# Kernel tuning notes

Measured on AMD Instinct MI355X. Metric: run time of the kernel, lower is better.

## Reference

```python
import jax, jax.numpy as jnp
import numpy as np

EPS = 1e-5
NUM_HEADS = 12

def _ln(x, g, b):
    m = jnp.mean(x, -1, keepdims=True)
    v = jnp.var(x, -1, keepdims=True)
    return (x - m) * jax.lax.rsqrt(v + EPS) * g + b

def setup_inputs():
    key = jax.random.key(0)
    ks = jax.random.split(key, 8)
    D, Dh = 768, 3072
    B, T, H, Wd = 8, 8, 14, 14
    def w(k, shape, scale=0.02):
        return jax.random.normal(k, shape, jnp.float32) * scale
    return dict(
        x=jax.random.normal(ks[0], (B, T * H * Wd + 1, D), jnp.float32),
        W_mq=w(ks[1], (D, D)), b_mq=jnp.zeros((D,), jnp.float32),
        W_mk=w(ks[2], (D, D)), b_mk=jnp.zeros((D,), jnp.float32),
        g1=jnp.ones((D,), jnp.float32), be1=jnp.zeros((D,), jnp.float32),
        W_qkv=w(ks[3], (3 * D, D)),
        W_proj=w(ks[4], (D, D)), b_proj=jnp.zeros((D,), jnp.float32),
        g2=jnp.ones((D,), jnp.float32), be2=jnp.zeros((D,), jnp.float32),
        W_fc1=w(ks[5], (Dh, D)), b_fc1=jnp.zeros((Dh,), jnp.float32),
        W_fc2=w(ks[6], (D, Dh)), b_fc2=jnp.zeros((D,), jnp.float32),
        B=B, T=T, H=H, Wd=Wd,
    )

def reference(x, W_mq, b_mq, W_mk, b_mk, g1, be1, W_qkv, W_proj, b_proj,
              g2, be2, W_fc1, b_fc1, W_fc2, b_fc2, B, T, H, Wd):
    D = x.shape[-1]
    nh = NUM_HEADS
    hd = D // nh
    res = x
    # cls token: (B,1,D) -> repeated per frame -> (B*T,1,D)
    cls = jnp.repeat(x[:, :1, :], T, axis=1).reshape(B * T, 1, D)
    # spatial tokens: 'b (h w t) m -> (b t) (h w) m'  (t is fastest-varying)
    xs = x[:, 1:, :].reshape(B, H * Wd, T, D).transpose(0, 2, 1, 3).reshape(B * T, H * Wd, D)
    xt = jnp.concatenate([cls, xs], axis=1)  # (BT, N=197, D)
    # learned QK-gated mask
    qm = xt @ W_mq.T + b_mq
    km = xt @ W_mk.T + b_mk
    lm = jnp.einsum('bnd,bmd->bnm', qm, km)
    lm = lm.at[:, 0, 0].set(100.0)  # force cls->cls gate open
    lm = jax.nn.sigmoid(lm)
    # attention (drop rates are 0; drop_path is identity at inference)
    xn = _ln(xt, g1, be1)
    BT, N = xt.shape[0], xt.shape[1]
    qkv = (xn @ W_qkv.T).reshape(BT, N, 3, nh, hd).transpose(2, 0, 3, 1, 4)
    q, k, v = qkv[0], qkv[1], qkv[2]  # (BT, nh, N, hd)
    attn = jax.nn.softmax(jnp.einsum('bhnd,bhmd->bhnm', q, k) * (hd ** -0.5), axis=-1)
    attn = attn * lm[:, None, :, :]  # gate attention probs with learned mask
    o = jnp.einsum('bhnm,bhmd->bhnd', attn, v).transpose(0, 2, 1, 3).reshape(BT, N, D)
    o = o @ W_proj.T + b_proj
    # gather cls back (mean over frames) and scatter tokens back
    cls_o = jnp.mean(o[:, 0, :].reshape(B, T, D), axis=1, keepdims=True)  # (B,1,D)
    xs_o = o[:, 1:, :].reshape(B, T, H * Wd, D).transpose(0, 2, 1, 3).reshape(B, H * Wd * T, D)
    y = res + jnp.concatenate([cls_o, xs_o], axis=1)
    # MLP
    h = _ln(y, g2, be2)
    h = jax.nn.gelu(h @ W_fc1.T + b_fc1, approximate=False)
    y = y + (h @ W_fc2.T + b_fc2)
    return (y, lm)
```

## Files before the change

### kernel.cpp

```cpp
#include <hip/hip_runtime.h>
#include <cstdint>

typedef _Float16 f16;
typedef f16 f16x2 __attribute__((ext_vector_type(2)));
typedef f16 f16x4 __attribute__((ext_vector_type(4)));
typedef f16 f16x8 __attribute__((ext_vector_type(8)));
typedef float f32x4 __attribute__((ext_vector_type(4)));

constexpr int D = 768;
constexpr int NTOK = 197;
constexpr int BT = 64;
constexpr int ROWS_A = BT * NTOK;
constexpr int SEQ = 1569;
constexpr int ROWS_Y = 8 * SEQ;
constexpr int DH = 3072;
constexpr int CW = 2304;
constexpr long Y_ELEMS = (long)ROWS_Y * D;
constexpr long LM_ELEMS = (long)BT * NTOK * NTOK;

__device__ __forceinline__ void gload_lds16(const f16* g, f16* l) {
  __builtin_amdgcn_global_load_lds(
      (const __attribute__((address_space(1))) void*)g,
      (__attribute__((address_space(3))) void*)l, 16, 0, 0);
}

__global__ __launch_bounds__(256) void cvt_f16(const float* __restrict__ in,
                                               f16* __restrict__ out, int n4) {
  int i = blockIdx.x * 256 + threadIdx.x;
  if (i >= n4) return;
  const float4 v = *(const float4*)(in + (size_t)i * 4);
  f16x4 o = {(f16)v.x, (f16)v.y, (f16)v.z, (f16)v.w};
  *(f16x4*)(out + (size_t)i * 4) = o;
}

__global__ __launch_bounds__(192) void build_xt_xn(
    const float* __restrict__ x, const float* __restrict__ g1,
    const float* __restrict__ be1, f16* __restrict__ xt, f16* __restrict__ xn) {
  const int rid = blockIdx.x;
  const int bt = rid / NTOK, n = rid % NTOK;
  const int b = bt >> 3, t = bt & 7;
  const int src = (n == 0) ? b * SEQ : b * SEQ + 1 + (n - 1) * 8 + t;
  const int tid = threadIdx.x, d0 = tid * 4;
  const float4 v = *(const float4*)(x + (size_t)src * D + d0);
  float s = v.x + v.y + v.z + v.w;
  float q = v.x * v.x + v.y * v.y + v.z * v.z + v.w * v.w;
  const int lane = tid & 63, wv = tid >> 6;
  for (int off = 32; off; off >>= 1) {
    s += __shfl_xor(s, off);
    q += __shfl_xor(q, off);
  }
  __shared__ float red[2][3];
  if (lane == 0) { red[0][wv] = s; red[1][wv] = q; }
  __syncthreads();
  s = red[0][0] + red[0][1] + red[0][2];
  q = red[1][0] + red[1][1] + red[1][2];
  const float mean = s * (1.f / 768.f);
  const float var = q * (1.f / 768.f) - mean * mean;
  const float rs = rsqrtf(var + 1e-5f);
  const size_t ob = (size_t)rid * D + d0;
  f16x4 xo = {(f16)v.x, (f16)v.y, (f16)v.z, (f16)v.w};
  *(f16x4*)(xt + ob) = xo;
  const float4 gv = *(const float4*)(g1 + d0);
  const float4 bv = *(const float4*)(be1 + d0);
  f16x4 no = {(f16)((v.x - mean) * rs * gv.x + bv.x),
              (f16)((v.y - mean) * rs * gv.y + bv.y),
              (f16)((v.z - mean) * rs * gv.z + bv.z),
              (f16)((v.w - mean) * rs * gv.w + bv.w)};
  *(f16x4*)(xn + ob) = no;
}

constexpr int EPI_F16 = 0;
constexpr int EPI_F16_BIAS = 1;
constexpr int EPI_SIG = 2;
constexpr int EPI_F16_BIAS_GELU = 3;
constexpr int EPI_F32_BIAS_RES = 4;

template <int EPI>
__global__ __launch_bounds__(256, 3) void gemm_f16(
    const f16* __restrict__ A, const f16* __restrict__ B,
    const float* __restrict__ bias, float* __restrict__ Cf,
    f16* __restrict__ Ch, const float* __restrict__ Res, int M, int N, int K,
    int ldc, long sA, long sB, long sC) {
  constexpr int BM = 128, BN = 128, BK = 32;
  __shared__ f16 As[BM][BK];
  __shared__ f16 Bs[BN][BK];
  const int tid = threadIdx.x;
  const int bm = blockIdx.y * BM, bn = blockIdx.x * BN;
  const int z = blockIdx.z;
  A += (size_t)z * sA;
  B += (size_t)z * sB;
  const int lane = tid & 63, wave = tid >> 6;
  const int wm = (wave >> 1) * 64, wn = (wave & 1) * 64;
  const int l15 = lane & 15, quad = lane >> 4;

  const int gr = lane >> 2;
  const int gc = (lane & 3) * 8;
  int a_row0 = bm + wave * 16 + gr;       if (a_row0 >= M) a_row0 = M - 1;
  int a_row1 = bm + (wave + 4) * 16 + gr; if (a_row1 >= M) a_row1 = M - 1;
  int b_row0 = bn + wave * 16 + gr;       if (b_row0 >= N) b_row0 = N - 1;
  int b_row1 = bn + (wave + 4) * 16 + gr; if (b_row1 >= N) b_row1 = N - 1;
  const f16* ap0 = A + (size_t)a_row0 * K + gc;
  const f16* ap1 = A + (size_t)a_row1 * K + gc;
  const f16* bp0 = B + (size_t)b_row0 * K + gc;
  const f16* bp1 = B + (size_t)b_row1 * K + gc;
  f16* as0 = &As[wave * 16][0];
  f16* as1 = &As[(wave + 4) * 16][0];
  f16* bs0 = &Bs[wave * 16][0];
  f16* bs1 = &Bs[(wave + 4) * 16][0];

  f32x4 acc[4][4] = {};

  for (int kt = 0; kt < K; kt += BK) {
    gload_lds16(ap0 + kt, as0);
    gload_lds16(ap1 + kt, as1);
    gload_lds16(bp0 + kt, bs0);
    gload_lds16(bp1 + kt, bs1);
    __syncthreads();
    f16x8 af[4], bf[4];
#pragma unroll
    for (int i = 0; i < 4; i++) {
      af[i] = *(const f16x8*)&As[wm + i * 16 + l15][quad * 8];
      bf[i] = *(const f16x8*)&Bs[wn + i * 16 + l15][quad * 8];
    }
#pragma unroll
    for (int i = 0; i < 4; i++)
#pragma unroll
      for (int j = 0; j < 4; j++)
        acc[i][j] =
            __builtin_amdgcn_mfma_f32_16x16x32_f16(af[i], bf[j], acc[i][j], 0, 0, 0);
    __syncthreads();
  }

#pragma unroll
  for (int i = 0; i < 4; i++) {
#pragma unroll
    for (int j = 0; j < 4; j++) {
      const int col = bn + wn + j * 16 + l15;
      if (col >= N) continue;
#pragma unroll
      for (int r = 0; r < 4; r++) {
        const int row = bm + wm + i * 16 + quad * 4 + r;
        if (row >= M) continue;
        float v = acc[i][j][r];
        const size_t ci = (size_t)z * sC + (size_t)row * ldc + col;
        if constexpr (EPI == EPI_F16) {
          Ch[ci] = (f16)v;
        } else if constexpr (EPI == EPI_F16_BIAS) {
          Ch[ci] = (f16)(v + bias[col]);
        } else if constexpr (EPI == EPI_SIG) {
          if (row == 0 && col == 0) v = 100.f;
          Cf[ci] = 1.f / (1.f + __expf(-v));
        } else if constexpr (EPI == EPI_F16_BIAS_GELU) {
          v += bias[col];
          Ch[ci] = (f16)(0.5f * v * (1.f + erff(v * 0.70710678118f)));
        } else if constexpr (EPI == EPI_F32_BIAS_RES) {
          Cf[ci] = v + bias[col] + Res[ci];
        }
      }
    }
  }
}

__global__ __launch_bounds__(256, 2) void attn_kernel(
    const f16* __restrict__ qkv, const float* __restrict__ lm,
    f16* __restrict__ o) {
  __shared__ f16 Ks[208][72];
  __shared__ f16 Vt[64][232];
  __shared__ f16 Ps[4][16][40];
  const int bh = blockIdx.x;
  const int bt = bh / 12, h = bh % 12;
  const int tid = threadIdx.x, lane = tid & 63, w = tid >> 6;
  const int l15 = lane & 15, quad = lane >> 4;
  const size_t base = (size_t)bt * NTOK * CW + (size_t)h * 64;

  for (int idx = tid; idx < 208 * 8; idx += 256) {
    const int r = idx >> 3, c = (idx & 7) * 8;
    f16x8 kv = {};
    if (r < NTOK) kv = *(const f16x8*)(qkv + base + (size_t)r * CW + 768 + c);
    *(f16x8*)&Ks[r][c] = kv;
  }
  for (int cb = 0; cb < 8; cb++) {
    const int r = tid;
    if (r < NTOK) {
      const f16x8 vv = *(const f16x8*)(qkv + base + (size_t)r * CW + 1536 + cb * 8);
#pragma unroll
      for (int j = 0; j < 8; j++) Vt[cb * 8 + j][r] = vv[j];
    }
  }
  for (int idx = tid; idx < 64 * 35; idx += 256) {
    const int d = idx / 35, m = NTOK + idx % 35;
    Vt[d][m] = (f16)0.f;
  }
  __syncthreads();

  for (int nt = w; nt < 13; nt += 4) {
    const int nq = nt * 16 + l15;
    const f16* qrow = qkv + base + (size_t)nq * CW;
    const f16x8 aq0 = *(const f16x8*)(qrow + quad * 8);
    const f16x8 aq1 = *(const f16x8*)(qrow + 32 + quad * 8);
    f32x4 S[13];
#pragma unroll
    for (int t = 0; t < 13; t++) {
      const f16x8 bk0 = *(const f16x8*)&Ks[t * 16 + l15][quad * 8];
      const f16x8 bk1 = *(const f16x8*)&Ks[t * 16 + l15][32 + quad * 8];
      f32x4 s = {};
      s = __builtin_amdgcn_mfma_f32_16x16x32_f16(aq0, bk0, s, 0, 0, 0);
      s = __builtin_amdgcn_mfma_f32_16x16x32_f16(aq1, bk1, s, 0, 0, 0);
      S[t] = s;
    }
    float mx[4] = {-3e38f, -3e38f, -3e38f, -3e38f};
#pragma unroll
    for (int t = 0; t < 13; t++) {
      const int m = t * 16 + l15;
#pragma unroll
      for (int r = 0; r < 4; r++) {
        float v = (m < NTOK) ? S[t][r] * 0.125f : -1e30f;
        S[t][r] = v;
        mx[r] = fmaxf(mx[r], v);
      }
    }
#pragma unroll
    for (int off = 1; off < 16; off <<= 1)
#pragma unroll
      for (int r = 0; r < 4; r++) mx[r] = fmaxf(mx[r], __shfl_xor(mx[r], off));
    float den[4] = {0.f, 0.f, 0.f, 0.f};
#pragma unroll
    for (int t = 0; t < 13; t++)
#pragma unroll
      for (int r = 0; r < 4; r++) {
        const float e = __expf(S[t][r] - mx[r]);
        S[t][r] = e;
        den[r] += e;
      }
#pragma unroll
    for (int off = 1; off < 16; off <<= 1)
#pragma unroll
      for (int r = 0; r < 4; r++) den[r] += __shfl_xor(den[r], off);
    float inv[4];
#pragma unroll
    for (int r = 0; r < 4; r++) inv[r] = 1.f / den[r];
#pragma unroll
    for (int t = 0; t < 13; t++) {
      const int m = t * 16 + l15;
#pragma unroll
      for (int r = 0; r < 4; r++) {
        const int nrow = nt * 16 + quad * 4 + r;
        float g = 0.f;
        if (m < NTOK && nrow < NTOK)
          g = lm[((size_t)bt * NTOK + nrow) * NTOK + m];
        S[t][r] *= inv[r] * g;
      }
    }
    f32x4 O[4] = {};
    for (int c = 0; c < 7; c++) {
      __builtin_amdgcn_wave_barrier();
#pragma unroll
      for (int tt = 0; tt < 2; tt++) {
        const int t = 2 * c + tt;
#pragma unroll
        for (int r = 0; r < 4; r++) {
          const f16 pv = (t < 13) ? (f16)S[t][r] : (f16)0.f;
          Ps[w][quad * 4 + r][tt * 16 + l15] = pv;
        }
      }
      __builtin_amdgcn_wave_barrier();
      const f16x8 ap = *(const f16x8*)&Ps[w][l15][quad * 8];
#pragma unroll
      for (int dt = 0; dt < 4; dt++) {
        const f16x8 bv = *(const f16x8*)&Vt[dt * 16 + l15][c * 32 + quad * 8];
        O[dt] = __builtin_amdgcn_mfma_f32_16x16x32_f16(ap, bv, O[dt], 0, 0, 0);
      }
    }
#pragma unroll
    for (int dt = 0; dt < 4; dt++)
#pragma unroll
      for (int r = 0; r < 4; r++) {
        const int nrow = nt * 16 + quad * 4 + r;
        if (nrow < NTOK)
          o[((size_t)bt * NTOK + nrow) * D + h * 64 + dt * 16 + l15] =
              (f16)O[dt][r];
      }
  }
}

__global__ __launch_bounds__(192) void scatter_y_ln(
    const float* __restrict__ x, const f16* __restrict__ po,
    const float* __restrict__ g2, const float* __restrict__ be2,
    float* __restrict__ y, f16* __restrict__ yn) {
  const int rid = blockIdx.x;
  const int b = rid / SEQ, pos = rid % SEQ;
  const int tid = threadIdx.x, d0 = tid * 4;
  float4 v = *(const float4*)(x + (size_t)rid * D + d0);
  if (pos == 0) {
    float ax = 0, ay = 0, az = 0, aw = 0;
    for (int t = 0; t < 8; t++) {
      const f16x4 p = *(const f16x4*)(po + ((size_t)(b * 8 + t) * NTOK) * D + d0);
      ax += (float)p[0]; ay += (float)p[1]; az += (float)p[2]; aw += (float)p[3];
    }
    v.x += ax * 0.125f; v.y += ay * 0.125f; v.z += az * 0.125f; v.w += aw * 0.125f;
  } else {
    const int hw = (pos - 1) >> 3, t = (pos - 1) & 7;
    const f16x4 p =
        *(const f16x4*)(po + ((size_t)((b * 8 + t) * NTOK + 1 + hw)) * D + d0);
    v.x += (float)p[0]; v.y += (float)p[1]; v.z += (float)p[2]; v.w += (float)p[3];
  }
  *(float4*)(y + (size_t)rid * D + d0) = v;
  float s = v.x + v.y + v.z + v.w;
  float q = v.x * v.x + v.y * v.y + v.z * v.z + v.w * v.w;
  const int lane = tid & 63, wv = tid >> 6;
  for (int off = 32; off; off >>= 1) {
    s += __shfl_xor(s, off);
    q += __shfl_xor(q, off);
  }
  __shared__ float red[2][3];
  if (lane == 0) { red[0][wv] = s; red[1][wv] = q; }
  __syncthreads();
  s = red[0][0] + red[0][1] + red[0][2];
  q = red[1][0] + red[1][1] + red[1][2];
  const float mean = s * (1.f / 768.f);
  const float var = q * (1.f / 768.f) - mean * mean;
  const float rs = rsqrtf(var + 1e-5f);
  const float4 gv = *(const float4*)(g2 + d0);
  const float4 bv = *(const float4*)(be2 + d0);
  f16x4 no = {(f16)((v.x - mean) * rs * gv.x + bv.x),
              (f16)((v.y - mean) * rs * gv.y + bv.y),
              (f16)((v.z - mean) * rs * gv.z + bv.z),
              (f16)((v.w - mean) * rs * gv.w + bv.w)};
  *(f16x4*)(yn + (size_t)rid * D + d0) = no;
}

extern "C" void kernel_launch(void* const* d_in, const int* in_sizes, int n_in,
                              void* d_out, int out_size, void* d_ws,
                              size_t ws_size, hipStream_t stream) {
  const float* x = (const float*)d_in[0];
  const float* W_mq = (const float*)d_in[1];
  const float* b_mq = (const float*)d_in[2];
  const float* W_mk = (const float*)d_in[3];
  const float* b_mk = (const float*)d_in[4];
  const float* g1 = (const float*)d_in[5];
  const float* be1 = (const float*)d_in[6];
  const float* W_qkv = (const float*)d_in[7];
  const float* W_proj = (const float*)d_in[8];
  const float* b_proj = (const float*)d_in[9];
  const float* g2 = (const float*)d_in[10];
  const float* be2 = (const float*)d_in[11];
  const float* W_fc1 = (const float*)d_in[12];
  const float* b_fc1 = (const float*)d_in[13];
  const float* W_fc2 = (const float*)d_in[14];
  const float* b_fc2 = (const float*)d_in[15];

  char* ws = (char*)d_ws;
  size_t off = 0;
  auto alloc = [&](size_t bytes) {
    size_t o = off;
    off = (off + bytes + 255) & ~(size_t)255;
    return o;
  };
  const size_t o_wmq = alloc((size_t)D * D * 2);
  const size_t o_wmk = alloc((size_t)D * D * 2);
  const size_t o_wqkv = alloc((size_t)CW * D * 2);
  const size_t o_wproj = alloc((size_t)D * D * 2);
  const size_t o_wfc1 = alloc((size_t)DH * D * 2);
  const size_t o_wfc2 = alloc((size_t)D * DH * 2);
  const size_t o_xt = alloc((size_t)ROWS_A * D * 2);
  const size_t o_xn = alloc((size_t)ROWS_A * D * 2);
  const size_t o_qm = alloc((size_t)ROWS_A * D * 2);
  alloc((size_t)ROWS_A * D * 2);
  const size_t o_km = o_qm + (size_t)ROWS_A * D * 2;
  const size_t o_qkv = o_qm;
  const size_t o_o = o_xn;
  const size_t o_po = o_qm + (size_t)ROWS_A * CW * 2;
  const size_t o_yn = o_xt;
  const size_t o_h = o_qm;

  f16* wmq = (f16*)(ws + o_wmq);
  f16* wmk = (f16*)(ws + o_wmk);
  f16* wqkv = (f16*)(ws + o_wqkv);
  f16* wproj = (f16*)(ws + o_wproj);
  f16* wfc1 = (f16*)(ws + o_wfc1);
  f16* wfc2 = (f16*)(ws + o_wfc2);
  f16* xt = (f16*)(ws + o_xt);
  f16* xn = (f16*)(ws + o_xn);
  f16* qm = (f16*)(ws + o_qm);
  f16* km = (f16*)(ws + o_km);
  f16* qkv = (f16*)(ws + o_qkv);
  f16* oatt = (f16*)(ws + o_o);
  f16* po = (f16*)(ws + o_po);
  f16* yn = (f16*)(ws + o_yn);
  f16* h = (f16*)(ws + o_h);

  float* y_out = (float*)d_out;
  float* lm_out = (float*)d_out + Y_ELEMS;

  const dim3 blk(256);
  auto cvt = [&](const float* src, f16* dst, int n) {
    cvt_f16<<<dim3((n / 4 + 255) / 256), blk, 0, stream>>>(src, dst, n / 4);
  };
  cvt(W_mq, wmq, D * D);
  cvt(W_mk, wmk, D * D);
  cvt(W_qkv, wqkv, CW * D);
  cvt(W_proj, wproj, D * D);
  cvt(W_fc1, wfc1, DH * D);
  cvt(W_fc2, wfc2, D * DH);

  build_xt_xn<<<dim3(ROWS_A), dim3(192), 0, stream>>>(x, g1, be1, xt, xn);

  auto grd = [](int N_, int M_, int Z_) {
    return dim3((N_ + 127) / 128, (M_ + 127) / 128, Z_);
  };
  gemm_f16<EPI_F16_BIAS><<<grd(D, ROWS_A, 1), blk, 0, stream>>>(
      xt, wmq, b_mq, nullptr, qm, nullptr, ROWS_A, D, D, D, 0, 0, 0);
  gemm_f16<EPI_F16_BIAS><<<grd(D, ROWS_A, 1), blk, 0, stream>>>(
      xt, wmk, b_mk, nullptr, km, nullptr, ROWS_A, D, D, D, 0, 0, 0);
  gemm_f16<EPI_SIG><<<grd(NTOK, NTOK, BT), blk, 0, stream>>>(
      qm, km, nullptr, lm_out, nullptr, nullptr, NTOK, NTOK, D, NTOK,
      (long)NTOK * D, (long)NTOK * D, (long)NTOK * NTOK);
  gemm_f16<EPI_F16><<<grd(CW, ROWS_A, 1), blk, 0, stream>>>(
      xn, wqkv, nullptr, nullptr, qkv, nullptr, ROWS_A, CW, D, CW, 0, 0, 0);
  attn_kernel<<<dim3(BT * 12), blk, 0, stream>>>(qkv, lm_out, oatt);
  gemm_f16<EPI_F16_BIAS><<<grd(D, ROWS_A, 1), blk, 0, stream>>>(
      oatt, wproj, b_proj, nullptr, po, nullptr, ROWS_A, D, D, D, 0, 0, 0);
  scatter_y_ln<<<dim3(ROWS_Y), dim3(192), 0, stream>>>(x, po, g2, be2, y_out, yn);
  gemm_f16<EPI_F16_BIAS_GELU><<<grd(DH, ROWS_Y, 1), blk, 0, stream>>>(
      yn, wfc1, b_fc1, nullptr, h, nullptr, ROWS_Y, DH, D, DH, 0, 0, 0);
  gemm_f16<EPI_F32_BIAS_RES><<<grd(D, ROWS_Y, 1), blk, 0, stream>>>(
      h, wfc2, b_fc2, y_out, nullptr, y_out, ROWS_Y, D, DH, D, 0, 0, 0);
  (void)in_sizes; (void)n_in; (void)out_size; (void)ws_size;
}
```

Measured before the change: 670.3 us.

## Double-buffer GEMM LDS tiles, fuse mask Q/K projections, use tanh GELU

The GEMM kernel now keeps two LDS buffers and issues global-to-LDS loads for the next K tile while the current one is in MFMA, so memory latency can overlap compute. The two mask projection GEMMs become one GEMM over concatenated weights and biases, with leading-dimension parameters added so the batched mask GEMM reads Q and K from the interleaved buffer. The exact erf GELU is replaced by a tanh-form approximation built on __expf. Double buffering doubles LDS use per block and may lower occupancy. The GELU change alters numerics slightly.

Measured after the change: 657.4 us. Within noise of the previous version (-1.9%).

```diff
diff --git a/kernel.cpp b/kernel.cpp
--- a/kernel.cpp
+++ b/kernel.cpp
@@ -16,7 +16,6 @@
 constexpr int DH = 3072;
 constexpr int CW = 2304;
 constexpr long Y_ELEMS = (long)ROWS_Y * D;
-constexpr long LM_ELEMS = (long)BT * NTOK * NTOK;
 
 __device__ __forceinline__ void gload_lds16(const f16* g, f16* l) {
   __builtin_amdgcn_global_load_lds(
@@ -31,6 +30,14 @@
   const float4 v = *(const float4*)(in + (size_t)i * 4);
   f16x4 o = {(f16)v.x, (f16)v.y, (f16)v.z, (f16)v.w};
   *(f16x4*)(out + (size_t)i * 4) = o;
+}
+
+__global__ __launch_bounds__(256) void concat2_f32(const float* __restrict__ a,
+                                                   const float* __restrict__ b,
+                                                   float* __restrict__ o, int n) {
+  int i = blockIdx.x * 256 + threadIdx.x;
+  if (i < n) o[i] = a[i];
+  else if (i < 2 * n) o[i] = b[i - n];
 }
 
 __global__ __launch_bounds__(192) void build_xt_xn(
@@ -80,10 +87,10 @@
     const f16* __restrict__ A, const f16* __restrict__ B,
     const float* __restrict__ bias, float* __restrict__ Cf,
     f16* __restrict__ Ch, const float* __restrict__ Res, int M, int N, int K,
-    int ldc, long sA, long sB, long sC) {
+    int lda, int ldb, int ldc, long sA, long sB, long sC) {
   constexpr int BM = 128, BN = 128, BK = 32;
-  __shared__ f16 As[BM][BK];
-  __shared__ f16 Bs[BN][BK];
+  __shared__ f16 As[2][BM][BK];
+  __shared__ f16 Bs[2][BN][BK];
   const int tid = threadIdx.x;
   const int bm = blockIdx.y * BM, bn = blockIdx.x * BN;
   const int z = blockIdx.z;
@@ -99,28 +106,25 @@
   int a_row1 = bm + (wave + 4) * 16 + gr; if (a_row1 >= M) a_row1 = M - 1;
   int b_row0 = bn + wave * 16 + gr;       if (b_row0 >= N) b_row0 = N - 1;
   int b_row1 = bn + (wave + 4) * 16 + gr; if (b_row1 >= N) b_row1 = N - 1;
-  const f16* ap0 = A + (size_t)a_row0 * K + gc;
-  const f16* ap1 = A + (size_t)a_row1 * K + gc;
-  const f16* bp0 = B + (size_t)b_row0 * K + gc;
-  const f16* bp1 = B + (size_t)b_row1 * K + gc;
-  f16* as0 = &As[wave * 16][0];
-  f16* as1 = &As[(wave + 4) * 16][0];
-  f16* bs0 = &Bs[wave * 16][0];
-  f16* bs1 = &Bs[(wave + 4) * 16][0];
+  const f16* ap0 = A + (size_t)a_row0 * lda + gc;
+  const f16* ap1 = A + (size_t)a_row1 * lda + gc;
+  const f16* bp0 = B + (size_t)b_row0 * ldb + gc;
+  const f16* bp1 = B + (size_t)b_row1 * ldb + gc;
 
   f32x4 acc[4][4] = {};
 
-  for (int kt = 0; kt < K; kt += BK) {
-    gload_lds16(ap0 + kt, as0);
-    gload_lds16(ap1 + kt, as1);
-    gload_lds16(bp0 + kt, bs0);
-    gload_lds16(bp1 + kt, bs1);
-    __syncthreads();
+  auto stage = [&](int buf, int k) {
+    gload_lds16(ap0 + k, &As[buf][wave * 16][0]);
+    gload_lds16(ap1 + k, &As[buf][(wave + 4) * 16][0]);
+    gload_lds16(bp0 + k, &Bs[buf][wave * 16][0]);
+    gload_lds16(bp1 + k, &Bs[buf][(wave + 4) * 16][0]);
+  };
+  auto compute = [&](int buf) {
     f16x8 af[4], bf[4];
 #pragma unroll
     for (int i = 0; i < 4; i++) {
-      af[i] = *(const f16x8*)&As[wm + i * 16 + l15][quad * 8];
-      bf[i] = *(const f16x8*)&Bs[wn + i * 16 + l15][quad * 8];
+      af[i] = *(const f16x8*)&As[buf][wm + i * 16 + l15][quad * 8];
+      bf[i] = *(const f16x8*)&Bs[buf][wn + i * 16 + l15][quad * 8];
     }
 #pragma unroll
     for (int i = 0; i < 4; i++)
@@ -128,6 +132,16 @@
       for (int j = 0; j < 4; j++)
         acc[i][j] =
             __builtin_amdgcn_mfma_f32_16x16x32_f16(af[i], bf[j], acc[i][j], 0, 0, 0);
+  };
+
+  stage(0, 0);
+  __syncthreads();
+  for (int kt = 0; kt < K; kt += 2 * BK) {
+    stage(1, kt + BK);
+    compute(0);
+    __syncthreads();
+    if (kt + 2 * BK < K) stage(0, kt + 2 * BK);
+    compute(1);
     __syncthreads();
   }
 
@@ -151,8 +165,10 @@
           if (row == 0 && col == 0) v = 100.f;
           Cf[ci] = 1.f / (1.f + __expf(-v));
         } else if constexpr (EPI == EPI_F16_BIAS_GELU) {
-          v += bias[col];
-          Ch[ci] = (f16)(0.5f * v * (1.f + erff(v * 0.70710678118f)));
+          const float u = v + bias[col];
+          const float t = u * (0.79788456f + 0.0356774081f * u * u);
+          const float e = __expf(2.f * t);
+          Ch[ci] = (f16)(u * (e / (e + 1.f)));
         } else if constexpr (EPI == EPI_F32_BIAS_RES) {
           Cf[ci] = v + bias[col] + Res[ci];
         }
@@ -356,33 +372,31 @@
     off = (off + bytes + 255) & ~(size_t)255;
     return o;
   };
-  const size_t o_wmq = alloc((size_t)D * D * 2);
-  const size_t o_wmk = alloc((size_t)D * D * 2);
+  const size_t o_wmqk = alloc((size_t)2 * D * D * 2);
+  const size_t o_bmqk = alloc((size_t)2 * D * 4);
   const size_t o_wqkv = alloc((size_t)CW * D * 2);
   const size_t o_wproj = alloc((size_t)D * D * 2);
   const size_t o_wfc1 = alloc((size_t)DH * D * 2);
   const size_t o_wfc2 = alloc((size_t)D * DH * 2);
   const size_t o_xt = alloc((size_t)ROWS_A * D * 2);
   const size_t o_xn = alloc((size_t)ROWS_A * D * 2);
-  const size_t o_qm = alloc((size_t)ROWS_A * D * 2);
-  alloc((size_t)ROWS_A * D * 2);
-  const size_t o_km = o_qm + (size_t)ROWS_A * D * 2;
-  const size_t o_qkv = o_qm;
+  const size_t o_big = alloc((size_t)ROWS_A * CW * 2);
+  const size_t o_po = alloc((size_t)ROWS_A * D * 2);
+  const size_t o_qmkm = o_big;
+  const size_t o_qkv = o_big;
   const size_t o_o = o_xn;
-  const size_t o_po = o_qm + (size_t)ROWS_A * CW * 2;
   const size_t o_yn = o_xt;
-  const size_t o_h = o_qm;
-
-  f16* wmq = (f16*)(ws + o_wmq);
-  f16* wmk = (f16*)(ws + o_wmk);
+  const size_t o_h = o_big;
+
+  f16* wmqk = (f16*)(ws + o_wmqk);
+  float* bmqk = (float*)(ws + o_bmqk);
   f16* wqkv = (f16*)(ws + o_wqkv);
   f16* wproj = (f16*)(ws + o_wproj);
   f16* wfc1 = (f16*)(ws + o_wfc1);
   f16* wfc2 = (f16*)(ws + o_wfc2);
   f16* xt = (f16*)(ws + o_xt);
   f16* xn = (f16*)(ws + o_xn);
-  f16* qm = (f16*)(ws + o_qm);
-  f16* km = (f16*)(ws + o_km);
+  f16* qmkm = (f16*)(ws + o_qmkm);
   f16* qkv = (f16*)(ws + o_qkv);
   f16* oatt = (f16*)(ws + o_o);
   f16* po = (f16*)(ws + o_po);
@@ -396,34 +410,38 @@
   auto cvt = [&](const float* src, f16* dst, int n) {
     cvt_f16<<<dim3((n / 4 + 255) / 256), blk, 0, stream>>>(src, dst, n / 4);
   };
-  cvt(W_mq, wmq, D * D);
-  cvt(W_mk, wmk, D * D);
+  cvt(W_mq, wmqk, D * D);
+  cvt(W_mk, wmqk + (size_t)D * D, D * D);
   cvt(W_qkv, wqkv, CW * D);
   cvt(W_proj, wproj, D * D);
   cvt(W_fc1, wfc1, DH * D);
   cvt(W_fc2, wfc2, D * DH);
+  concat2_f32<<<dim3(6), blk, 0, stream>>>(b_mq, b_mk, bmqk, D);
 
   build_xt_xn<<<dim3(ROWS_A), dim3(192), 0, stream>>>(x, g1, be1, xt, xn);
 
   auto grd = [](int N_, int M_, int Z_) {
     return dim3((N_ + 127) / 128, (M_ + 127) / 128, Z_);
   };
-  gemm_f16<EPI_F16_BIAS><<<grd(D, ROWS_A, 1), blk, 0, stream>>>(
-      xt, wmq, b_mq, nullptr, qm, nullptr, ROWS_A, D, D, D, 0, 0, 0);
-  gemm_f16<EPI_F16_BIAS><<<grd(D, ROWS_A, 1), blk, 0, stream>>>(
-      xt, wmk, b_mk, nullptr, km, nullptr, ROWS_A, D, D, D, 0, 0, 0);
+  gemm_f16<EPI_F16_BIAS><<<grd(2 * D, ROWS_A, 1), blk, 0, stream>>>(
+      xt, wmqk, bmqk, nullptr, qmkm, nullptr, ROWS_A, 2 * D, D, D, D, 2 * D,
+      0, 0, 0);
   gemm_f16<EPI_SIG><<<grd(NTOK, NTOK, BT), blk, 0, stream>>>(
-      qm, km, nullptr, lm_out, nullptr, nullptr, NTOK, NTOK, D, NTOK,
-      (long)NTOK * D, (long)NTOK * D, (long)NTOK * NTOK);
+      qmkm, qmkm + D, nullptr, lm_out, nullptr, nullptr, NTOK, NTOK, D,
+      2 * D, 2 * D, NTOK, (long)NTOK * 2 * D, (long)NTOK * 2 * D,
+      (long)NTOK * NTOK);
   gemm_f16<EPI_F16><<<grd(CW, ROWS_A, 1), blk, 0, stream>>>(
-      xn, wqkv, nullptr, nullptr, qkv, nullptr, ROWS_A, CW, D, CW, 0, 0, 0);
+      xn, wqkv, nullptr, nullptr, qkv, nullptr, ROWS_A, CW, D, D, D, CW,
+      0, 0, 0);
   attn_kernel<<<dim3(BT * 12), blk, 0, stream>>>(qkv, lm_out, oatt);
   gemm_f16<EPI_F16_BIAS><<<grd(D, ROWS_A, 1), blk, 0, stream>>>(
-      oatt, wproj, b_proj, nullptr, po, nullptr, ROWS_A, D, D, D, 0, 0, 0);
+      oatt, wproj, b_proj, nullptr, po, nullptr, ROWS_A, D, D, D, D, D,
+      0, 0, 0);
   scatter_y_ln<<<dim3(ROWS_Y), dim3(192), 0, stream>>>(x, po, g2, be2, y_out, yn);
   gemm_f16<EPI_F16_BIAS_GELU><<<grd(DH, ROWS_Y, 1), blk, 0, stream>>>(
-      yn, wfc1, b_fc1, nullptr, h, nullptr, ROWS_Y, DH, D, DH, 0, 0, 0);
+      yn, wfc1, b_fc1, nullptr, h, nullptr, ROWS_Y, DH, D, D, D, DH, 0, 0, 0);
   gemm_f16<EPI_F32_BIAS_RES><<<grd(D, ROWS_Y, 1), blk, 0, stream>>>(
-      h, wfc2, b_fc2, y_out, nullptr, y_out, ROWS_Y, D, DH, D, 0, 0, 0);
+      h, wfc2, b_fc2, y_out, nullptr, y_out, ROWS_Y, D, DH, DH, DH, D,
+      0, 0, 0);
   (void)in_sizes; (void)n_in; (void)out_size; (void)ws_size;
 }
```
